# Kernel tuning notes

Measured on AMD Instinct MI355X. Metric: run time of the kernel, lower is better.

## Reference

```python
import jax, jax.numpy as jnp
import numpy as np

# Module config (from init_kwargs): causal=False, window_size=(256,256), window_type=0,
# softmax_scale=None -> 1/sqrt(D), dropout=0 (eval mode).
WINDOW_LEFT, WINDOW_RIGHT = 256, 256


def _window_mask(Sq, Sk, causal, use_window_mask):
    """Boolean [Sq, Sk] visibility mask, FA2 semantics (right-aligned offset)."""
    qi = jnp.arange(Sq)[:, None]
    kj = jnp.arange(Sk)[None, :]
    offset = Sk - Sq
    if causal:
        return kj <= qi + offset  # window (-1, 0)
    if use_window_mask:
        m = jnp.ones((Sq, Sk), dtype=bool)
        if WINDOW_LEFT >= 0:
            m = m & (kj >= qi + offset - WINDOW_LEFT)
        if WINDOW_RIGHT >= 0:
            m = m & (kj <= qi + offset + WINDOW_RIGHT)
        return m
    return None  # full attention


def setup_inputs() -> dict:
    key = jax.random.key(0)
    kq, kkv = jax.random.split(key)
    B, Sq, Sk, H, D = 2, 2048, 2048, 16, 64
    q = jax.random.normal(kq, (B, Sq, H, D), dtype=jnp.float32)
    kv = jax.random.normal(kkv, (B, Sk, 2, H, D), dtype=jnp.float32)
    return {"q": q, "kv": kv, "causal": 0, "use_window_mask": 1, "return_attn_probs": 0}


def reference(q, kv, causal, use_window_mask, return_attn_probs):
    # q: (B, Sq, H, D); kv: (B, Sk, 2, H, D)
    B, Sq, H, D = q.shape
    Sk = kv.shape[1]
    k = kv[:, :, 0]  # (B, Sk, H, D)
    v = kv[:, :, 1]
    scale = 1.0 / (D ** 0.5)
    scores = jnp.einsum('bqhd,bkhd->bhqk', q, k) * scale  # (B, H, Sq, Sk)
    mask = _window_mask(Sq, Sk, bool(causal), bool(use_window_mask))
    if mask is not None:
        scores = jnp.where(mask[None, None], scores, jnp.finfo(scores.dtype).min)
    probs = jax.nn.softmax(scores, axis=-1)
    out = jnp.einsum('bhqk,bkhd->bqhd', probs, v)  # (B, Sq, H, D)
    return out
```

## Files before the change

kernel.cpp:

```cpp
#include <hip/hip_runtime.h>
#include <hip/hip_bf16.h>

#define B_    2
#define SQ_   2048
#define SK_   2048
#define NH_   16
#define DH_   64
#define WIN_  256
#define NEG_  -30000.0f

typedef __bf16 bf16_t;
typedef bf16_t bf16x8 __attribute__((ext_vector_type(8)));
typedef bf16_t bf16x4 __attribute__((ext_vector_type(4)));
typedef float  f32x4  __attribute__((ext_vector_type(4)));
typedef float  f32x16 __attribute__((ext_vector_type(16)));

#define KSTRIDE 72
#define VSTRIDE 72
#define PSTRIDE 72

static __device__ __forceinline__ f32x16 zero16() {
  f32x16 z;
#pragma unroll
  for (int i = 0; i < 16; ++i) z[i] = 0.f;
  return z;
}

__global__ __launch_bounds__(256, 2)
void fa_fwd(const float* __restrict__ qg, const float* __restrict__ kvg,
            float* __restrict__ outg) {
  const int tid  = threadIdx.x;
  const int wid  = tid >> 6;
  const int lane = tid & 63;
  const int c31  = lane & 31;
  const int hi   = lane >> 5;

  const int bid = blockIdx.x;
  const int qb  = bid >> 5;
  const int bh  = bid & 31;
  const int b   = bh >> 4;
  const int h   = bh & 15;

  const int q0b = qb * 128;
  const int q0  = q0b + wid * 32;

  __shared__ __align__(16) bf16_t sK [2][64 * KSTRIDE];
  __shared__ __align__(16) bf16_t sVT[2][64 * VSTRIDE];
  __shared__ __align__(16) bf16_t sP [4][32 * PSTRIDE];
  bf16_t* plw = sP[wid];

  const float qscale = 0.125f * 1.44269504088896340736f;
  const float* qrow = qg + ((size_t)((b * SQ_ + q0 + c31) * NH_ + h)) * DH_;
  bf16x8 qfrag[4];
#pragma unroll
  for (int ds = 0; ds < 4; ++ds) {
    const int d0 = ds * 16 + hi * 8;
    f32x4 a0 = *(const f32x4*)(qrow + d0);
    f32x4 a1 = *(const f32x4*)(qrow + d0 + 4);
#pragma unroll
    for (int i = 0; i < 4; ++i) {
      qfrag[ds][i]     = (bf16_t)(a0[i] * qscale);
      qfrag[ds][i + 4] = (bf16_t)(a1[i] * qscale);
    }
  }

  f32x16 oacc[2];
  oacc[0] = zero16(); oacc[1] = zero16();
  float m = NEG_, el = 0.f;

  int klo = q0b - WIN_; if (klo < 0) klo = 0;
  int khi = q0b + 127 + WIN_ + 1; if (khi > SK_) khi = SK_;
  const int nt = (khi - klo + 63) >> 6;

  const float* kbase = kvg + (size_t)b * SK_ * 2 * NH_ * DH_ + (size_t)h * DH_;
  const float* vbase = kbase + NH_ * DH_;
  const size_t krow_stride = 2 * NH_ * DH_;

  const int skey = tid >> 2;
  const int sd0  = (tid & 3) * 16;

  f32x4 ka[4], va[4];

  auto issue_loads = [&](int kt) {
    const float* kr = kbase + (size_t)(kt + skey) * krow_stride + sd0;
    const float* vr = vbase + (size_t)(kt + skey) * krow_stride + sd0;
#pragma unroll
    for (int i = 0; i < 4; ++i) {
      ka[i] = *(const f32x4*)(kr + 4 * i);
      va[i] = *(const f32x4*)(vr + 4 * i);
    }
  };

  auto stage = [&](int bb) {
#pragma unroll
    for (int hh = 0; hh < 2; ++hh) {
      bf16x8 wk;
#pragma unroll
      for (int i = 0; i < 4; ++i) {
        wk[i] = (bf16_t)ka[2 * hh][i]; wk[i + 4] = (bf16_t)ka[2 * hh + 1][i];
      }
      *(bf16x8*)(&sK[bb][skey * KSTRIDE + sd0 + 8 * hh]) = wk;
      const int dbase = sd0 + 8 * hh;
      const int vcol  = skey ^ (((dbase >> 3) & 7) << 3);
#pragma unroll
      for (int i = 0; i < 4; ++i) {
        sVT[bb][(dbase + i)     * VSTRIDE + vcol] = (bf16_t)va[2 * hh][i];
        sVT[bb][(dbase + 4 + i) * VSTRIDE + vcol] = (bf16_t)va[2 * hh + 1][i];
      }
    }
  };

  issue_loads(klo);
  stage(0);
  if (nt > 1) issue_loads(klo + 64);
  __syncthreads();

  int buf = 0;
  for (int t = 0; t < nt; ++t) {
    const int kk = klo + t * 64;
    if (t + 1 < nt) stage(buf ^ 1);
    if (t + 2 < nt) issue_loads(klo + (t + 2) * 64);

    if (kk + 63 >= q0 - WIN_ && kk <= q0 + 31 + WIN_) {
      f32x16 sc[2];
      __builtin_amdgcn_s_setprio(1);
#pragma unroll
      for (int kh = 0; kh < 2; ++kh) {
        f32x16 acc = zero16();
#pragma unroll
        for (int ds = 0; ds < 4; ++ds) {
          bf16x8 kf = *(const bf16x8*)(
              &sK[buf][(kh * 32 + c31) * KSTRIDE + ds * 16 + hi * 8]);
          acc = __builtin_amdgcn_mfma_f32_32x32x16_bf16(kf, qfrag[ds], acc, 0, 0, 0);
        }
        sc[kh] = acc;
      }
      __builtin_amdgcn_s_setprio(0);

      if (kk < q0 - 225 || kk > q0 + 193) {
        const int qa = q0 + c31;
#pragma unroll
        for (int kh = 0; kh < 2; ++kh)
#pragma unroll
          for (int r = 0; r < 16; ++r) {
            int key = kk + kh * 32 + (r & 3) + 8 * (r >> 2) + 4 * hi;
            unsigned dd = (unsigned)(key - qa + WIN_);
            if (dd > 2u * WIN_) sc[kh][r] = NEG_;
          }
      }

      float tl = NEG_;
#pragma unroll
      for (int kh = 0; kh < 2; ++kh)
#pragma unroll
        for (int r = 0; r < 16; r += 4)
          tl = fmaxf(tl, fmaxf(fmaxf(sc[kh][r], sc[kh][r + 1]),
                               fmaxf(sc[kh][r + 2], sc[kh][r + 3])));

      const bool defer = (__all(tl <= m + 8.0f) != 0);
      float mnew = m;
      if (!defer) {
        float tr = fmaxf(tl, __shfl_xor(tl, 32));
        mnew = fmaxf(m, tr);
      }

      float psum = 0.f;
#pragma unroll
      for (int kh = 0; kh < 2; ++kh)
#pragma unroll
        for (int g = 0; g < 4; ++g) {
          float p0 = exp2f(sc[kh][4 * g + 0] - mnew);
          float p1 = exp2f(sc[kh][4 * g + 1] - mnew);
          float p2 = exp2f(sc[kh][4 * g + 2] - mnew);
          float p3 = exp2f(sc[kh][4 * g + 3] - mnew);
          psum += (p0 + p1) + (p2 + p3);
          bf16x4 pk;
          pk[0] = (bf16_t)p0; pk[1] = (bf16_t)p1;
          pk[2] = (bf16_t)p2; pk[3] = (bf16_t)p3;
          *(bf16x4*)(&plw[c31 * PSTRIDE + kh * 32 + g * 8 + hi * 4]) = pk;
        }

      if (!defer) {
        const float alq = exp2f(m - mnew);
#pragma unroll
        for (int r = 0; r < 16; ++r) {
          const int row = (r & 3) + 8 * (r >> 2) + 4 * hi;
          const float al = __shfl(alq, row);
          oacc[0][r] *= al; oacc[1][r] *= al;
        }
        el = el * alq + psum;
        m = mnew;
      } else {
        el += psum;
      }

      asm volatile("s_waitcnt lgkmcnt(0)" ::: "memory");

      bf16x8 pf[4];
#pragma unroll
      for (int ks = 0; ks < 4; ++ks)
        pf[ks] = *(const bf16x8*)(&plw[c31 * PSTRIDE + ks * 16 + hi * 8]);

      __builtin_amdgcn_s_setprio(1);
#pragma unroll
      for (int dt = 0; dt < 2; ++dt) {
        const int d  = dt * 32 + c31;
        const int c8 = ((d >> 3) & 7) << 3;
#pragma unroll
        for (int ks = 0; ks < 4; ++ks) {
          bf16x8 vf = *(const bf16x8*)(
              &sVT[buf][d * VSTRIDE + ((ks * 16 + hi * 8) ^ c8)]);
          oacc[dt] = __builtin_amdgcn_mfma_f32_32x32x16_bf16(pf[ks], vf, oacc[dt], 0, 0, 0);
        }
      }
      __builtin_amdgcn_s_setprio(0);
    }

    __syncthreads();
    buf ^= 1;
  }

  el += __shfl_xor(el, 32);
  const float rlq = 1.0f / el;
#pragma unroll
  for (int r = 0; r < 16; ++r) {
    const int row = (r & 3) + 8 * (r >> 2) + 4 * hi;
    const float rl = __shfl(rlq, row);
    float* orow = outg + ((size_t)((b * SQ_ + q0 + row) * NH_ + h)) * DH_;
#pragma unroll
    for (int dt = 0; dt < 2; ++dt)
      orow[dt * 32 + c31] = oacc[dt][r] * rl;
  }
}

extern "C" void kernel_launch(void* const* d_in, const int* in_sizes, int n_in,
                              void* d_out, int out_size, void* d_ws, size_t ws_size,
                              hipStream_t stream) {
  (void)in_sizes; (void)n_in; (void)out_size; (void)d_ws; (void)ws_size;
  const float* q  = (const float*)d_in[0];
  const float* kv = (const float*)d_in[1];
  float* out = (float*)d_out;
  dim3 grid(B_ * NH_ * (SQ_ / 128));
  fa_fwd<<<grid, 256, 0, stream>>>(q, kv, out);
}
```

Before: 116.8 us.

## Pre-convert KV to swizzled bf16 workspace and stage tiles via async global-to-LDS loads

Adds a prep kernel that converts K and V from fp32 to bf16 once, writing K in an XOR-swizzled row layout and V transposed into a workspace buffer. The attention kernel then loads each tile directly into LDS with global_load_lds, which removes the per-tile register conversion, scattered transpose stores and repeated fp32 reads of overlapping window tiles. The cost is an extra kernel launch and a workspace round trip. The pipeline also drops from a two-tile register prefetch to a single async prefetch.

```diff
diff --git a/kernel.cpp b/kernel.cpp
--- a/kernel.cpp
+++ b/kernel.cpp
@@ -14,10 +14,16 @@
 typedef bf16_t bf16x4 __attribute__((ext_vector_type(4)));
 typedef float  f32x4  __attribute__((ext_vector_type(4)));
 typedef float  f32x16 __attribute__((ext_vector_type(16)));
-
-#define KSTRIDE 72
-#define VSTRIDE 72
+typedef unsigned int u32;
+
+#define KE_BH 131072
+#define VT_E  4194304
 #define PSTRIDE 72
+
+#define GLOAD_LDS16(g, l)                                                      \
+  __builtin_amdgcn_global_load_lds(                                            \
+      (const __attribute__((address_space(1))) u32*)(g),                       \
+      (__attribute__((address_space(3))) u32*)(l), 16, 0, 0)
 
 static __device__ __forceinline__ f32x16 zero16() {
   f32x16 z;
@@ -26,8 +32,55 @@
   return z;
 }
 
+__global__ __launch_bounds__(256)
+void kv_prep(const float* __restrict__ kvg, bf16_t* __restrict__ wse) {
+  __shared__ __align__(16) bf16_t sT[4096];
+  const int tid = threadIdx.x;
+  const int bb  = blockIdx.x;
+  const int bh  = bb >> 5, kt = bb & 31;
+  const int b   = bh >> 4, h = bh & 15;
+
+  const int skey = tid >> 2;
+  const int sd0  = (tid & 3) * 16;
+  const int key  = kt * 64 + skey;
+
+  const float* src =
+      kvg + ((((size_t)b * SK_ + key) * 2) * NH_ + h) * (size_t)DH_ + sd0;
+  f32x4 ka[4], va[4];
+#pragma unroll
+  for (int i = 0; i < 4; ++i) {
+    ka[i] = *(const f32x4*)(src + 4 * i);
+    va[i] = *(const f32x4*)(src + NH_ * DH_ + 4 * i);
+  }
+
+  bf16_t* kdst = wse + (size_t)bh * KE_BH + (size_t)key * 64;
+#pragma unroll
+  for (int hh = 0; hh < 2; ++hh) {
+    bf16x8 w;
+#pragma unroll
+    for (int i = 0; i < 4; ++i) {
+      w[i] = (bf16_t)ka[2 * hh][i]; w[i + 4] = (bf16_t)ka[2 * hh + 1][i];
+    }
+    const int c = (sd0 >> 3) + hh;
+    *(bf16x8*)(kdst + ((c ^ (key & 7)) << 3)) = w;
+  }
+
+  const int g = skey >> 3, kw = skey & 7;
+#pragma unroll
+  for (int j = 0; j < 16; ++j) {
+    const int d = sd0 + j;
+    sT[d * 64 + ((g ^ (d & 7)) << 3) + kw] = (bf16_t)va[j >> 2][j & 3];
+  }
+  __syncthreads();
+
+  const int dr = tid >> 2, rp = (tid & 3) * 16;
+  bf16_t* vdst = wse + VT_E + (size_t)bh * KE_BH + (size_t)dr * 2048 + kt * 64 + rp;
+  *(bf16x8*)(vdst)     = *(const bf16x8*)(&sT[dr * 64 + rp]);
+  *(bf16x8*)(vdst + 8) = *(const bf16x8*)(&sT[dr * 64 + rp + 8]);
+}
+
 __global__ __launch_bounds__(256, 2)
-void fa_fwd(const float* __restrict__ qg, const float* __restrict__ kvg,
+void fa_fwd(const float* __restrict__ qg, const bf16_t* __restrict__ wse,
             float* __restrict__ outg) {
   const int tid  = threadIdx.x;
   const int wid  = tid >> 6;
@@ -44,10 +97,13 @@
   const int q0b = qb * 128;
   const int q0  = q0b + wid * 32;
 
-  __shared__ __align__(16) bf16_t sK [2][64 * KSTRIDE];
-  __shared__ __align__(16) bf16_t sVT[2][64 * VSTRIDE];
-  __shared__ __align__(16) bf16_t sP [4][32 * PSTRIDE];
+  __shared__ __align__(16) bf16_t sK[2][4096];
+  __shared__ __align__(16) bf16_t sV[2][4096];
+  __shared__ __align__(16) bf16_t sP[4][32 * PSTRIDE];
   bf16_t* plw = sP[wid];
+
+  const bf16_t* kbh = wse + (size_t)bh * KE_BH;
+  const bf16_t* vbh = wse + VT_E + (size_t)bh * KE_BH;
 
   const float qscale = 0.125f * 1.44269504088896340736f;
   const float* qrow = qg + ((size_t)((b * SQ_ + q0 + c31) * NH_ + h)) * DH_;
@@ -72,65 +128,36 @@
   int khi = q0b + 127 + WIN_ + 1; if (khi > SK_) khi = SK_;
   const int nt = (khi - klo + 63) >> 6;
 
-  const float* kbase = kvg + (size_t)b * SK_ * 2 * NH_ * DH_ + (size_t)h * DH_;
-  const float* vbase = kbase + NH_ * DH_;
-  const size_t krow_stride = 2 * NH_ * DH_;
-
-  const int skey = tid >> 2;
-  const int sd0  = (tid & 3) * 16;
-
-  f32x4 ka[4], va[4];
-
-  auto issue_loads = [&](int kt) {
-    const float* kr = kbase + (size_t)(kt + skey) * krow_stride + sd0;
-    const float* vr = vbase + (size_t)(kt + skey) * krow_stride + sd0;
-#pragma unroll
-    for (int i = 0; i < 4; ++i) {
-      ka[i] = *(const f32x4*)(kr + 4 * i);
-      va[i] = *(const f32x4*)(vr + 4 * i);
-    }
+  const int tid8 = tid * 8;
+  const int vs0  = (tid >> 3) * 2048 + (tid & 7) * 8;
+
+  auto stage_async = [&](int kt, bf16_t* kd, bf16_t* vd) {
+    GLOAD_LDS16(kbh + kt * 64 + tid8,        kd + tid8);
+    GLOAD_LDS16(kbh + kt * 64 + 2048 + tid8, kd + 2048 + tid8);
+    GLOAD_LDS16(vbh + kt + vs0,              vd + tid8);
+    GLOAD_LDS16(vbh + kt + vs0 + 65536,      vd + 2048 + tid8);
   };
 
-  auto stage = [&](int bb) {
-#pragma unroll
-    for (int hh = 0; hh < 2; ++hh) {
-      bf16x8 wk;
-#pragma unroll
-      for (int i = 0; i < 4; ++i) {
-        wk[i] = (bf16_t)ka[2 * hh][i]; wk[i + 4] = (bf16_t)ka[2 * hh + 1][i];
-      }
-      *(bf16x8*)(&sK[bb][skey * KSTRIDE + sd0 + 8 * hh]) = wk;
-      const int dbase = sd0 + 8 * hh;
-      const int vcol  = skey ^ (((dbase >> 3) & 7) << 3);
-#pragma unroll
-      for (int i = 0; i < 4; ++i) {
-        sVT[bb][(dbase + i)     * VSTRIDE + vcol] = (bf16_t)va[2 * hh][i];
-        sVT[bb][(dbase + 4 + i) * VSTRIDE + vcol] = (bf16_t)va[2 * hh + 1][i];
-      }
-    }
-  };
-
-  issue_loads(klo);
-  stage(0);
-  if (nt > 1) issue_loads(klo + 64);
+  stage_async(klo, sK[0], sV[0]);
   __syncthreads();
 
   int buf = 0;
   for (int t = 0; t < nt; ++t) {
     const int kk = klo + t * 64;
-    if (t + 1 < nt) stage(buf ^ 1);
-    if (t + 2 < nt) issue_loads(klo + (t + 2) * 64);
+    if (t + 1 < nt) stage_async(kk + 64, sK[buf ^ 1], sV[buf ^ 1]);
 
     if (kk + 63 >= q0 - WIN_ && kk <= q0 + 31 + WIN_) {
       f32x16 sc[2];
       __builtin_amdgcn_s_setprio(1);
 #pragma unroll
       for (int kh = 0; kh < 2; ++kh) {
+        const int key = kh * 32 + c31;
+        const int sw  = key & 7;
         f32x16 acc = zero16();
 #pragma unroll
         for (int ds = 0; ds < 4; ++ds) {
           bf16x8 kf = *(const bf16x8*)(
-              &sK[buf][(kh * 32 + c31) * KSTRIDE + ds * 16 + hi * 8]);
+              &sK[buf][key * 64 + (((ds * 2 + hi) ^ sw) << 3)]);
           acc = __builtin_amdgcn_mfma_f32_32x32x16_bf16(kf, qfrag[ds], acc, 0, 0, 0);
         }
         sc[kh] = acc;
@@ -205,11 +232,11 @@
 #pragma unroll
       for (int dt = 0; dt < 2; ++dt) {
         const int d  = dt * 32 + c31;
-        const int c8 = ((d >> 3) & 7) << 3;
+        const int sw = d & 7;
 #pragma unroll
         for (int ks = 0; ks < 4; ++ks) {
           bf16x8 vf = *(const bf16x8*)(
-              &sVT[buf][d * VSTRIDE + ((ks * 16 + hi * 8) ^ c8)]);
+              &sV[buf][d * 64 + (((ks * 2 + hi) ^ sw) << 3)]);
           oacc[dt] = __builtin_amdgcn_mfma_f32_32x32x16_bf16(pf[ks], vf, oacc[dt], 0, 0, 0);
         }
       }
@@ -236,10 +263,12 @@
 extern "C" void kernel_launch(void* const* d_in, const int* in_sizes, int n_in,
                               void* d_out, int out_size, void* d_ws, size_t ws_size,
                               hipStream_t stream) {
-  (void)in_sizes; (void)n_in; (void)out_size; (void)d_ws; (void)ws_size;
+  (void)in_sizes; (void)n_in; (void)out_size; (void)ws_size;
   const float* q  = (const float*)d_in[0];
   const float* kv = (const float*)d_in[1];
   float* out = (float*)d_out;
-  dim3 grid(B_ * NH_ * (SQ_ / 128));
-  fa_fwd<<<grid, 256, 0, stream>>>(q, kv, out);
-}
+  bf16_t* wse = (bf16_t*)d_ws;
+
+  kv_prep<<<dim3(32 * 32), 256, 0, stream>>>(kv, wse);
+  fa_fwd<<<dim3(B_ * NH_ * (SQ_ / 128)), 256, 0, stream>>>(q, wse, out);
+}
```

Measured after the change: 122.9 us. 5.3% more time.
